# Kernel tuning notes

Hardware: AMD Instinct MI355X
Metric: run time of the kernel (lower is better)

Reference implementation:

```python
import jax, jax.numpy as jnp
import numpy as np

SPATIAL_DILATIONS = [1, 4, 16]
TEMPORAL_DILATIONS = [1, 2]


def setup_inputs() -> dict:
    key = jax.random.key(0)
    k1, k2, k3 = jax.random.split(key, 3)
    B, C, T, H, W = 4, 64, 16, 128, 128
    u = jax.random.normal(k1, (B, C, T, H, W), dtype=jnp.float32)
    # module initializes these to constants 0.1 / 0.05; use small random values
    D_spatial = jnp.full((len(SPATIAL_DILATIONS), C), 0.1, dtype=jnp.float32) \
        + 0.01 * jax.random.normal(k2, (len(SPATIAL_DILATIONS), C), dtype=jnp.float32)
    D_temporal = jnp.full((len(TEMPORAL_DILATIONS), C), 0.05, dtype=jnp.float32) \
        + 0.01 * jax.random.normal(k3, (len(TEMPORAL_DILATIONS), C), dtype=jnp.float32)
    return {"u": u, "D_spatial": D_spatial, "D_temporal": D_temporal}


def _lap2d(u, d):
    """5-tap dilated 2D Laplacian with replicate (edge) padding.

    Equivalent to F.pad(mode='replicate') + depthwise conv2d with the
    sparse 3x3 cross kernel, applied over the last two dims of u.
    """
    h, w = u.shape[-2], u.shape[-1]
    p = jnp.pad(u, ((0, 0), (0, 0), (0, 0), (d, d), (d, d)), mode='edge')
    return (p[..., 0:h,        d:d + w]      # up
            + p[..., 2 * d:2 * d + h, d:d + w]  # down
            + p[..., d:d + h,  0:w]          # left
            + p[..., d:d + h,  2 * d:2 * d + w]  # right
            - 4.0 * u)


def reference(u, D_spatial, D_temporal):
    # signed_diffusion=False -> coeff = softplus(param)
    cs = jax.nn.softplus(D_spatial)   # (n_sd, C)
    ct = jax.nn.softplus(D_temporal)  # (n_td, C)
    t = u.shape[2]

    out = jnp.zeros_like(u)
    # spatial diffusion: sum over dilations of coeff * Laplacian
    for i, d in enumerate(SPATIAL_DILATIONS):
        out = out + cs[i][None, :, None, None, None] * _lap2d(u, d)

    # temporal diffusion (causal backward difference): u_past - u
    for i, dt in enumerate(TEMPORAL_DILATIONS):
        u_past = jnp.pad(u, ((0, 0), (0, 0), (dt, 0), (0, 0), (0, 0)),
                         mode='edge')[:, :, :t]
        out = out + ct[i][None, :, None, None, None] * (u_past - u)
    return out
```

## Files before the change

kernel.cpp:

```cpp
#include <hip/hip_runtime.h>
#include <math.h>

#define BB 4
#define CC 64
#define TT 16
#define HH 128
#define WW 128
#define HALO 16
#define PW (WW + 2*HALO)

typedef float f32x4 __attribute__((ext_vector_type(4)));

__device__ __forceinline__ float softplus_f(float x) {
    return (x > 20.0f) ? x : log1pf(expf(x));
}

__device__ __forceinline__ void barrier_lgkm() {
    asm volatile("s_waitcnt lgkmcnt(0)\n\ts_barrier" ::: "memory");
}

__global__ __launch_bounds__(1024, 4) void lap_st_kernel(
    const float* __restrict__ u,
    const float* __restrict__ Ds,
    const float* __restrict__ Dt,
    float* __restrict__ out)
{
    __shared__ __align__(16) float sm[HH * PW];

    const int bc = blockIdx.x;
    const int c  = bc & (CC - 1);
    const int tid = threadIdx.x;

    const float cs0 = softplus_f(Ds[0 * CC + c]);
    const float cs1 = softplus_f(Ds[1 * CC + c]);
    const float cs2 = softplus_f(Ds[2 * CC + c]);
    const float ct0 = softplus_f(Dt[0 * CC + c]);
    const float ct1 = softplus_f(Dt[1 * CC + c]);
    const float cu = -4.0f * (cs0 + cs1 + cs2) - (ct0 + ct1);

    const size_t bc_off = (size_t)bc * TT * (HH * WW);

    float4 nxt[4], cur[4], pm1[4], pm2[4];

    {
        const float4* up4 = (const float4*)(u + bc_off);
        #pragma unroll
        for (int i = 0; i < 4; ++i) cur[i] = up4[tid + (i << 10)];
        #pragma unroll
        for (int i = 0; i < 4; ++i) { pm1[i] = cur[i]; pm2[i] = cur[i]; }
    }

    for (int t = 0; t < TT; ++t) {
        f32x4* out4 = (f32x4*)(out + bc_off + (size_t)t * (HH * WW));

        barrier_lgkm();

        if (t < TT - 1) {
            const float4* up4 = (const float4*)(u + bc_off + (size_t)(t + 1) * (HH * WW));
            #pragma unroll
            for (int i = 0; i < 4; ++i) nxt[i] = up4[tid + (i << 10)];
        }

        #pragma unroll
        for (int i = 0; i < 4; ++i) {
            const int k = tid + (i << 10);
            const float4 v = cur[i];
            const int row  = k >> 5;
            const int colc = k & 31;
            *(float4*)&sm[row * PW + HALO + (colc << 2)] = v;
            if (colc == 0) {
                float4 s = make_float4(v.x, v.x, v.x, v.x);
                float* hp = &sm[row * PW];
                *(float4*)&hp[0] = s; *(float4*)&hp[4] = s;
                *(float4*)&hp[8] = s; *(float4*)&hp[12] = s;
            } else if (colc == 31) {
                float4 s = make_float4(v.w, v.w, v.w, v.w);
                float* hp = &sm[row * PW + HALO + WW];
                *(float4*)&hp[0] = s; *(float4*)&hp[4] = s;
                *(float4*)&hp[8] = s; *(float4*)&hp[12] = s;
            }
        }

        barrier_lgkm();

        #pragma unroll
        for (int i = 0; i < 4; ++i) {
            const int k   = tid + (i << 10);
            const int row = k >> 5;
            const int col = (k & 31) << 2;
            const float* rp = &sm[row * PW + HALO];

            const int rU1  = (row >= 1)       ? row - 1  : 0;
            const int rD1  = (row <= HH - 2)  ? row + 1  : HH - 1;
            const int rU4  = (row >= 4)       ? row - 4  : 0;
            const int rD4  = (row <= HH - 5)  ? row + 4  : HH - 1;
            const int rU16 = (row >= 16)      ? row - 16 : 0;
            const int rD16 = (row <= HH - 17) ? row + 16 : HH - 1;

            const float4 c0   = cur[i];
            const float4 vu1  = *(const float4*)&sm[rU1  * PW + HALO + col];
            const float4 vd1  = *(const float4*)&sm[rD1  * PW + HALO + col];
            const float4 vu4  = *(const float4*)&sm[rU4  * PW + HALO + col];
            const float4 vd4  = *(const float4*)&sm[rD4  * PW + HALO + col];
            const float4 vu16 = *(const float4*)&sm[rU16 * PW + HALO + col];
            const float4 vd16 = *(const float4*)&sm[rD16 * PW + HALO + col];
            const float4 l4   = *(const float4*)&rp[col - 4];
            const float4 r4   = *(const float4*)&rp[col + 4];
            const float4 l16  = *(const float4*)&rp[col - 16];
            const float4 r16  = *(const float4*)&rp[col + 16];

            const float4 p1 = pm1[i];
            const float4 p2 = pm2[i];

            f32x4 o;
            o.x = cs0 * (vu1.x + vd1.x + l4.w + c0.y)
                + cs1 * (vu4.x + vd4.x + l4.x + r4.x)
                + cs2 * (vu16.x + vd16.x + l16.x + r16.x)
                + cu * c0.x + ct0 * p1.x + ct1 * p2.x;
            o.y = cs0 * (vu1.y + vd1.y + c0.x + c0.z)
                + cs1 * (vu4.y + vd4.y + l4.y + r4.y)
                + cs2 * (vu16.y + vd16.y + l16.y + r16.y)
                + cu * c0.y + ct0 * p1.y + ct1 * p2.y;
            o.z = cs0 * (vu1.z + vd1.z + c0.y + c0.w)
                + cs1 * (vu4.z + vd4.z + l4.z + r4.z)
                + cs2 * (vu16.z + vd16.z + l16.z + r16.z)
                + cu * c0.z + ct0 * p1.z + ct1 * p2.z;
            o.w = cs0 * (vu1.w + vd1.w + c0.z + r4.x)
                + cs1 * (vu4.w + vd4.w + l4.w + r4.w)
                + cs2 * (vu16.w + vd16.w + l16.w + r16.w)
                + cu * c0.w + ct0 * p1.w + ct1 * p2.w;

            __builtin_nontemporal_store(o, &out4[k]);
        }

        if (t < TT - 1) {
            #pragma unroll
            for (int i = 0; i < 4; ++i) { pm2[i] = pm1[i]; pm1[i] = cur[i]; cur[i] = nxt[i]; }
        }
    }
}

extern "C" void kernel_launch(void* const* d_in, const int* in_sizes, int n_in,
                              void* d_out, int out_size, void* d_ws, size_t ws_size,
                              hipStream_t stream) {
    const float* u  = (const float*)d_in[0];
    const float* Ds = (const float*)d_in[1];
    const float* Dt = (const float*)d_in[2];
    float* out = (float*)d_out;

    const int nblocks = BB * CC;
    lap_st_kernel<<<dim3(nblocks), dim3(1024), 0, stream>>>(u, Ds, Dt, out);
}
```

Baseline: 121.1 us.

## Split each plane into 32-row strips with 16-row halos across more blocks

Each (batch, channel) plane is now split into four 32-row strips, each handled by a 256-thread block that also loads 16-row halos above and below. The launch grows from 256 to 1024 blocks, which should fill the GPU's CUs better and cut per-block shared memory. The cost is redundant halo traffic, since each strip reads 64 rows to produce 32, roughly doubling global reads of u.

```diff
diff --git a/kernel.cpp b/kernel.cpp
--- a/kernel.cpp
+++ b/kernel.cpp
@@ -6,8 +6,11 @@
 #define TT 16
 #define HH 128
 #define WW 128
+#define HW (HH*WW)
 #define HALO 16
 #define PW (WW + 2*HALO)
+#define QROWS 32
+#define LROWS 64
 
 typedef float f32x4 __attribute__((ext_vector_type(4)));
 
@@ -19,16 +22,19 @@
     asm volatile("s_waitcnt lgkmcnt(0)\n\ts_barrier" ::: "memory");
 }
 
-__global__ __launch_bounds__(1024, 4) void lap_st_kernel(
+__global__ __launch_bounds__(256, 4) void lap_st_kernel(
     const float* __restrict__ u,
     const float* __restrict__ Ds,
     const float* __restrict__ Dt,
     float* __restrict__ out)
 {
-    __shared__ __align__(16) float sm[HH * PW];
+    __shared__ __align__(16) float sm[LROWS * PW];
 
-    const int bc = blockIdx.x;
-    const int c  = bc & (CC - 1);
+    const int bid = blockIdx.x;
+    const int sh  = bid >> 8;
+    const int bc  = bid & 255;
+    const int c   = bc & (CC - 1);
+    const int R0  = sh << 5;
     const int tid = threadIdx.x;
 
     const float cs0 = softplus_f(Ds[0 * CC + c]);
@@ -38,46 +44,82 @@
     const float ct1 = softplus_f(Dt[1 * CC + c]);
     const float cu = -4.0f * (cs0 + cs1 + cs2) - (ct0 + ct1);
 
-    const size_t bc_off = (size_t)bc * TT * (HH * WW);
+    const size_t bc_off = (size_t)bc * TT * HW;
 
-    float4 nxt[4], cur[4], pm1[4], pm2[4];
+    const int bl = 16 - R0;
+    const int bh = 143 - R0;
+
+    float4 cur[4], nxt[4], pm1[4], pm2[4], hal[4];
 
     {
-        const float4* up4 = (const float4*)(u + bc_off);
+        const float* up = u + bc_off;
         #pragma unroll
-        for (int i = 0; i < 4; ++i) cur[i] = up4[tid + (i << 10)];
+        for (int i = 0; i < 4; ++i) {
+            const int k  = tid + (i << 8);
+            const int gr = R0 + (k >> 5);
+            cur[i] = *(const float4*)(up + gr * WW + ((k & 31) << 2));
+        }
+        #pragma unroll
+        for (int i = 0; i < 4; ++i) {
+            const int k    = tid + (i << 8);
+            const int j    = k >> 5;
+            const int slot = (j < 16) ? j : j + 32;
+            int gr = R0 - 16 + slot;
+            gr = (gr < 0) ? 0 : ((gr > 127) ? 127 : gr);
+            hal[i] = *(const float4*)(up + gr * WW + ((k & 31) << 2));
+        }
         #pragma unroll
         for (int i = 0; i < 4; ++i) { pm1[i] = cur[i]; pm2[i] = cur[i]; }
     }
 
     for (int t = 0; t < TT; ++t) {
-        f32x4* out4 = (f32x4*)(out + bc_off + (size_t)t * (HH * WW));
+        const float* up_nxt = u + bc_off + (size_t)(t + 1) * HW;
+        f32x4* outp = (f32x4*)(out + bc_off + (size_t)t * HW);
 
         barrier_lgkm();
 
-        if (t < TT - 1) {
-            const float4* up4 = (const float4*)(u + bc_off + (size_t)(t + 1) * (HH * WW));
-            #pragma unroll
-            for (int i = 0; i < 4; ++i) nxt[i] = up4[tid + (i << 10)];
-        }
-
         #pragma unroll
         for (int i = 0; i < 4; ++i) {
-            const int k = tid + (i << 10);
+            const int k    = tid + (i << 8);
+            const int lr   = 16 + (k >> 5);
+            const int colc = k & 31;
             const float4 v = cur[i];
-            const int row  = k >> 5;
-            const int colc = k & 31;
-            *(float4*)&sm[row * PW + HALO + (colc << 2)] = v;
+            *(float4*)&sm[lr * PW + HALO + (colc << 2)] = v;
             if (colc == 0) {
                 float4 s = make_float4(v.x, v.x, v.x, v.x);
-                float* hp = &sm[row * PW];
+                float* hp = &sm[lr * PW];
                 *(float4*)&hp[0] = s; *(float4*)&hp[4] = s;
                 *(float4*)&hp[8] = s; *(float4*)&hp[12] = s;
             } else if (colc == 31) {
                 float4 s = make_float4(v.w, v.w, v.w, v.w);
-                float* hp = &sm[row * PW + HALO + WW];
+                float* hp = &sm[lr * PW + HALO + WW];
                 *(float4*)&hp[0] = s; *(float4*)&hp[4] = s;
                 *(float4*)&hp[8] = s; *(float4*)&hp[12] = s;
+            }
+        }
+        #pragma unroll
+        for (int i = 0; i < 4; ++i) {
+            const int k    = tid + (i << 8);
+            const int j    = k >> 5;
+            const int slot = (j < 16) ? j : j + 32;
+            *(float4*)&sm[slot * PW + HALO + ((k & 31) << 2)] = hal[i];
+        }
+
+        if (t < TT - 1) {
+            #pragma unroll
+            for (int i = 0; i < 4; ++i) {
+                const int k  = tid + (i << 8);
+                const int gr = R0 + (k >> 5);
+                nxt[i] = *(const float4*)(up_nxt + gr * WW + ((k & 31) << 2));
+            }
+            #pragma unroll
+            for (int i = 0; i < 4; ++i) {
+                const int k    = tid + (i << 8);
+                const int j    = k >> 5;
+                const int slot = (j < 16) ? j : j + 32;
+                int gr = R0 - 16 + slot;
+                gr = (gr < 0) ? 0 : ((gr > 127) ? 127 : gr);
+                hal[i] = *(const float4*)(up_nxt + gr * WW + ((k & 31) << 2));
             }
         }
 
@@ -85,17 +127,18 @@
 
         #pragma unroll
         for (int i = 0; i < 4; ++i) {
-            const int k   = tid + (i << 10);
-            const int row = k >> 5;
-            const int col = (k & 31) << 2;
-            const float* rp = &sm[row * PW + HALO];
+            const int k    = tid + (i << 8);
+            const int lr   = 16 + (k >> 5);
+            const int colc = k & 31;
+            const int col  = colc << 2;
+            const float* rp = &sm[lr * PW + HALO];
 
-            const int rU1  = (row >= 1)       ? row - 1  : 0;
-            const int rD1  = (row <= HH - 2)  ? row + 1  : HH - 1;
-            const int rU4  = (row >= 4)       ? row - 4  : 0;
-            const int rD4  = (row <= HH - 5)  ? row + 4  : HH - 1;
-            const int rU16 = (row >= 16)      ? row - 16 : 0;
-            const int rD16 = (row <= HH - 17) ? row + 16 : HH - 1;
+            const int rU1  = (lr - 1  > bl) ? lr - 1  : bl;
+            const int rD1  = (lr + 1  < bh) ? lr + 1  : bh;
+            const int rU4  = (lr - 4  > bl) ? lr - 4  : bl;
+            const int rD4  = (lr + 4  < bh) ? lr + 4  : bh;
+            const int rU16 = (lr - 16 > bl) ? lr - 16 : bl;
+            const int rD16 = (lr + 16 < bh) ? lr + 16 : bh;
 
             const float4 c0   = cur[i];
             const float4 vu1  = *(const float4*)&sm[rU1  * PW + HALO + col];
@@ -130,7 +173,8 @@
                 + cs2 * (vu16.w + vd16.w + l16.w + r16.w)
                 + cu * c0.w + ct0 * p1.w + ct1 * p2.w;
 
-            __builtin_nontemporal_store(o, &out4[k]);
+            const int gr = R0 + (k >> 5);
+            __builtin_nontemporal_store(o, &outp[gr * 32 + colc]);
         }
 
         if (t < TT - 1) {
@@ -148,6 +192,6 @@
     const float* Dt = (const float*)d_in[2];
     float* out = (float*)d_out;
 
-    const int nblocks = BB * CC;
-    lap_st_kernel<<<dim3(nblocks), dim3(1024), 0, stream>>>(u, Ds, Dt, out);
+    const int nblocks = 4 * BB * CC;
+    lap_st_kernel<<<dim3(nblocks), dim3(256), 0, stream>>>(u, Ds, Dt, out);
 }
```

Measured after the change: 343.8 us. 184% more time.

## Double-buffer LDS tile and prefetch two timesteps ahead, dropping halo padding

Applied to the files above, without the earlier changes.

Stores the next timestep's plane into an alternate LDS buffer so each timestep needs one barrier instead of two, and adds a second register prefetch stage loading u two steps ahead. The padded halo columns are removed; edge replication is done with clamped indices and selects against the row's edge values. This hides global load latency and barrier stalls, at the cost of more LDS (128KB per block), more registers, and extra select logic.

```diff
diff --git a/kernel.cpp b/kernel.cpp
--- a/kernel.cpp
+++ b/kernel.cpp
@@ -6,8 +6,8 @@
 #define TT 16
 #define HH 128
 #define WW 128
-#define HALO 16
-#define PW (WW + 2*HALO)
+#define HW (HH*WW)
+#define PW 128
 
 typedef float f32x4 __attribute__((ext_vector_type(4)));
 
@@ -19,16 +19,18 @@
     asm volatile("s_waitcnt lgkmcnt(0)\n\ts_barrier" ::: "memory");
 }
 
+__device__ __forceinline__ float4 splat4(float v) { return make_float4(v, v, v, v); }
+
 __global__ __launch_bounds__(1024, 4) void lap_st_kernel(
     const float* __restrict__ u,
     const float* __restrict__ Ds,
     const float* __restrict__ Dt,
     float* __restrict__ out)
 {
-    __shared__ __align__(16) float sm[HH * PW];
+    __shared__ __align__(16) float sm[2 * HH * PW];
 
-    const int bc = blockIdx.x;
-    const int c  = bc & (CC - 1);
+    const int bc  = blockIdx.x;
+    const int c   = bc & (CC - 1);
     const int tid = threadIdx.x;
 
     const float cs0 = softplus_f(Ds[0 * CC + c]);
@@ -38,57 +40,53 @@
     const float ct1 = softplus_f(Dt[1 * CC + c]);
     const float cu = -4.0f * (cs0 + cs1 + cs2) - (ct0 + ct1);
 
-    const size_t bc_off = (size_t)bc * TT * (HH * WW);
+    const size_t bc_off = (size_t)bc * TT * HW;
 
-    float4 nxt[4], cur[4], pm1[4], pm2[4];
+    float4 cur[4], nxt[4], nn[4], pm1[4], pm2[4];
 
     {
-        const float4* up4 = (const float4*)(u + bc_off);
+        const float4* p0 = (const float4*)(u + bc_off);
         #pragma unroll
-        for (int i = 0; i < 4; ++i) cur[i] = up4[tid + (i << 10)];
+        for (int i = 0; i < 4; ++i) cur[i] = p0[tid + (i << 10)];
         #pragma unroll
-        for (int i = 0; i < 4; ++i) { pm1[i] = cur[i]; pm2[i] = cur[i]; }
+        for (int i = 0; i < 4; ++i) {
+            const int k = tid + (i << 10);
+            *(float4*)&sm[(k >> 5) * PW + ((k & 31) << 2)] = cur[i];
+            pm1[i] = cur[i]; pm2[i] = cur[i];
+        }
+        const float4* p1 = (const float4*)(u + bc_off + HW);
+        #pragma unroll
+        for (int i = 0; i < 4; ++i) nxt[i] = p1[tid + (i << 10)];
     }
 
     for (int t = 0; t < TT; ++t) {
-        f32x4* out4 = (f32x4*)(out + bc_off + (size_t)t * (HH * WW));
+        const int p = t & 1;
+        float* __restrict__ smA = &sm[p * (HH * PW)];
+        float* __restrict__ smB = &sm[(1 - p) * (HH * PW)];
+        f32x4* outp = (f32x4*)(out + bc_off + (size_t)t * HW);
 
         barrier_lgkm();
 
         if (t < TT - 1) {
-            const float4* up4 = (const float4*)(u + bc_off + (size_t)(t + 1) * (HH * WW));
             #pragma unroll
-            for (int i = 0; i < 4; ++i) nxt[i] = up4[tid + (i << 10)];
+            for (int i = 0; i < 4; ++i) {
+                const int k = tid + (i << 10);
+                *(float4*)&smB[(k >> 5) * PW + ((k & 31) << 2)] = nxt[i];
+            }
+        }
+
+        if (t < TT - 2) {
+            const float4* pn = (const float4*)(u + bc_off + (size_t)(t + 2) * HW);
+            #pragma unroll
+            for (int i = 0; i < 4; ++i) nn[i] = pn[tid + (i << 10)];
         }
 
         #pragma unroll
         for (int i = 0; i < 4; ++i) {
-            const int k = tid + (i << 10);
-            const float4 v = cur[i];
+            const int k    = tid + (i << 10);
             const int row  = k >> 5;
-            const int colc = k & 31;
-            *(float4*)&sm[row * PW + HALO + (colc << 2)] = v;
-            if (colc == 0) {
-                float4 s = make_float4(v.x, v.x, v.x, v.x);
-                float* hp = &sm[row * PW];
-                *(float4*)&hp[0] = s; *(float4*)&hp[4] = s;
-                *(float4*)&hp[8] = s; *(float4*)&hp[12] = s;
-            } else if (colc == 31) {
-                float4 s = make_float4(v.w, v.w, v.w, v.w);
-                float* hp = &sm[row * PW + HALO + WW];
-                *(float4*)&hp[0] = s; *(float4*)&hp[4] = s;
-                *(float4*)&hp[8] = s; *(float4*)&hp[12] = s;
-            }
-        }
-
-        barrier_lgkm();
-
-        #pragma unroll
-        for (int i = 0; i < 4; ++i) {
-            const int k   = tid + (i << 10);
-            const int row = k >> 5;
-            const int col = (k & 31) << 2;
-            const float* rp = &sm[row * PW + HALO];
+            const int col  = (k & 31) << 2;
+            const float* rp = &smA[row * PW];
 
             const int rU1  = (row >= 1)       ? row - 1  : 0;
             const int rD1  = (row <= HH - 2)  ? row + 1  : HH - 1;
@@ -98,16 +96,23 @@
             const int rD16 = (row <= HH - 17) ? row + 16 : HH - 1;
 
             const float4 c0   = cur[i];
-            const float4 vu1  = *(const float4*)&sm[rU1  * PW + HALO + col];
-            const float4 vd1  = *(const float4*)&sm[rD1  * PW + HALO + col];
-            const float4 vu4  = *(const float4*)&sm[rU4  * PW + HALO + col];
-            const float4 vd4  = *(const float4*)&sm[rD4  * PW + HALO + col];
-            const float4 vu16 = *(const float4*)&sm[rU16 * PW + HALO + col];
-            const float4 vd16 = *(const float4*)&sm[rD16 * PW + HALO + col];
-            const float4 l4   = *(const float4*)&rp[col - 4];
-            const float4 r4   = *(const float4*)&rp[col + 4];
-            const float4 l16  = *(const float4*)&rp[col - 16];
-            const float4 r16  = *(const float4*)&rp[col + 16];
+            const float4 vu1  = *(const float4*)&smA[rU1  * PW + col];
+            const float4 vd1  = *(const float4*)&smA[rD1  * PW + col];
+            const float4 vu4  = *(const float4*)&smA[rU4  * PW + col];
+            const float4 vd4  = *(const float4*)&smA[rD4  * PW + col];
+            const float4 vu16 = *(const float4*)&smA[rU16 * PW + col];
+            const float4 vd16 = *(const float4*)&smA[rD16 * PW + col];
+
+            const float e0   = rp[0];
+            const float e127 = rp[WW - 1];
+            const float4 l4r  = *(const float4*)&rp[(col >= 4)   ? col - 4  : 0];
+            const float4 r4r  = *(const float4*)&rp[(col <= 120) ? col + 4  : 120];
+            const float4 l16r = *(const float4*)&rp[(col >= 16)  ? col - 16 : 0];
+            const float4 r16r = *(const float4*)&rp[(col <= 108) ? col + 16 : 108];
+            const float4 l4  = (col >= 4)   ? l4r  : splat4(e0);
+            const float4 r4  = (col <= 120) ? r4r  : splat4(e127);
+            const float4 l16 = (col >= 16)  ? l16r : splat4(e0);
+            const float4 r16 = (col <= 108) ? r16r : splat4(e127);
 
             const float4 p1 = pm1[i];
             const float4 p2 = pm2[i];
@@ -130,12 +135,14 @@
                 + cs2 * (vu16.w + vd16.w + l16.w + r16.w)
                 + cu * c0.w + ct0 * p1.w + ct1 * p2.w;
 
-            __builtin_nontemporal_store(o, &out4[k]);
+            __builtin_nontemporal_store(o, &outp[k]);
         }
 
         if (t < TT - 1) {
             #pragma unroll
-            for (int i = 0; i < 4; ++i) { pm2[i] = pm1[i]; pm1[i] = cur[i]; cur[i] = nxt[i]; }
+            for (int i = 0; i < 4; ++i) {
+                pm2[i] = pm1[i]; pm1[i] = cur[i]; cur[i] = nxt[i]; nxt[i] = nn[i];
+            }
         }
     }
 }
```

New measurement: 270.1 us. +123.0%, slower.
